# Optimization experiments

Measured on AMD Instinct MI355X. Metric: run time of the kernel, lower is better.

Reference implementation:

```python
import jax, jax.numpy as jnp
import numpy as np

HIDDEN_DIM = 128
ATTN_DIM = 64
B, N = 2, 512

def setup_inputs() -> dict:
    key = jax.random.key(0)
    ks = jax.random.split(key, 8)
    s = 0.05
    return {
        "X":    jax.random.normal(ks[0], (B, N, HIDDEN_DIM), dtype=jnp.float32),
        "Wo":   jax.random.normal(ks[1], (ATTN_DIM, HIDDEN_DIM), dtype=jnp.float32) * s,
        "W1":   jax.random.normal(ks[2], (ATTN_DIM, HIDDEN_DIM), dtype=jnp.float32) * s,
        "Wphi": jax.random.normal(ks[3], (ATTN_DIM,), dtype=jnp.float32) * s,
        "Wy":   jax.random.normal(ks[4], (HIDDEN_DIM, HIDDEN_DIM), dtype=jnp.float32) * s,
        "by":   jax.random.normal(ks[5], (HIDDEN_DIM,), dtype=jnp.float32) * s,
        "We":   jax.random.normal(ks[6], (HIDDEN_DIM, ATTN_DIM), dtype=jnp.float32) * s,
        "be":   jax.random.normal(ks[7], (HIDDEN_DIM,), dtype=jnp.float32) * s,
    }

def reference(X, Wo, W1, Wphi, Wy, by, We, be):
    # h_o, h_1: [B, N, A]
    h_o = jnp.einsum('bnc,ac->bna', X, Wo)
    h_1 = jnp.einsum('bnc,ac->bna', X, W1)
    # pairwise tanh edge features e_ij: [B, N, N, A]
    e = jnp.tanh(h_o[:, :, None, :] + h_1[:, None, :, :])
    # scores [B, N, N] via w_phi projection, row-wise softmax over j
    scores = jnp.einsum('bija,a->bij', e, Wphi)
    alpha = jax.nn.softmax(scores, axis=-1)
    # value path 1: Wy x_j -> aggregated by alpha (bmm)
    X_y = jnp.einsum('bnc,hc->bnh', X, Wy) + by
    part1 = jnp.einsum('bij,bjh->bih', alpha, X_y)
    # value path 2: We e_ij -> weighted sum over j
    eval_ = jnp.einsum('bija,ha->bijh', e, We) + be  # [B, N, N, H]
    part2 = jnp.einsum('bij,bijh->bih', alpha, eval_)
    return part1 + part2
```

## Files before the change

kernel.cpp:

```cpp
#include <hip/hip_runtime.h>

#define B_ 2
#define N_ 512
#define C_ 128
#define A_ 64
#define H_ 128

#define SC2L 2.885390081777927f
#define NEG2LE -2.885390081777927f

#define OFF_WOT 0
#define OFF_W1T (OFF_WOT + C_*A_)
#define OFF_WYT (OFF_W1T + C_*A_)
#define OFF_WET (OFF_WYT + C_*H_)
#define OFF_V   (OFF_WET + A_*H_)
#define OFF_UT2 (OFF_V   + B_*N_*A_)
#define OFF_USP (OFF_UT2 + B_*N_*A_/2)
#define OFF_XYP (OFF_USP + B_*N_*A_/2)

__device__ __forceinline__ float fexp2(float x) { return __builtin_amdgcn_exp2f(x); }
__device__ __forceinline__ float frcp(float x)  { return __builtin_amdgcn_rcpf(x); }
__device__ __forceinline__ unsigned f2bf(float x) {
  unsigned u = __float_as_uint(x);
  return (u + 0x7fffu + ((u >> 16) & 1u)) >> 16;
}
__device__ __forceinline__ float bf_lo(unsigned d) { return __uint_as_float(d << 16); }
__device__ __forceinline__ float bf_hi(unsigned d) { return __uint_as_float(d & 0xffff0000u); }

__global__ __launch_bounds__(256) void prep_weights(
    const float* __restrict__ Wo, const float* __restrict__ W1,
    const float* __restrict__ Wy, const float* __restrict__ We,
    float* __restrict__ ws) {
  int t = blockIdx.x * 256 + threadIdx.x;
  if (t < A_*C_) {
    int a = t / C_, c = t % C_;
    ws[OFF_WOT + c*A_ + a] = Wo[t];
    ws[OFF_W1T + c*A_ + a] = W1[t];
    int h2 = t / A_, a2 = t % A_;
    ws[OFF_WET + a2*H_ + h2] = We[t];
  }
  if (t < H_*C_) {
    int h = t / C_, c = t % C_;
    ws[OFF_WYT + c*H_ + h] = Wy[t];
  }
}

__global__ __launch_bounds__(256) void proj_kernel(
    const float* __restrict__ X, const float* __restrict__ by,
    float* __restrict__ ws) {
  __shared__ float xs[2*C_];
  int row0 = blockIdx.x * 2;
  int t = threadIdx.x;
  if (t < 2*C_) xs[t] = X[(size_t)row0*C_ + t];
  __syncthreads();

  const float* wt;
  int col, stride;
  if (t < 64)       { wt = ws + OFF_WOT; col = t;       stride = A_; }
  else if (t < 128) { wt = ws + OFF_W1T; col = t - 64;  stride = A_; }
  else              { wt = ws + OFF_WYT; col = t - 128; stride = H_; }

  float acc0 = 0.f, acc1 = 0.f;
  #pragma unroll 8
  for (int c = 0; c < C_; ++c) {
    float wv = wt[c*stride + col];
    acc0 = fmaf(xs[c], wv, acc0);
    acc1 = fmaf(xs[C_ + c], wv, acc1);
  }

  int b = row0 >> 9, n0 = row0 & (N_-1);
  int k = n0 >> 1;

  if (t < 64) {
    float* o = ws + OFF_V + (size_t)row0*A_ + col;
    o[0] = fexp2(SC2L * acc0);
    o[A_] = fexp2(SC2L * acc1);
  } else if (t < 128) {
    int a = col;
    unsigned u0 = f2bf(fexp2(SC2L * acc0));
    unsigned u1 = f2bf(fexp2(SC2L * acc1));
    unsigned* usp = (unsigned*)(ws + OFF_USP);
    usp[(size_t)(b*(N_/2) + k)*A_ + a] = u0 | (u1 << 16);
    unsigned short* ut = (unsigned short*)(ws + OFF_UT2);
    size_t base = ((size_t)(b*(A_/2) + (a >> 1))*N_ + n0)*2 + (a & 1);
    ut[base] = (unsigned short)u0;
    ut[base + 2] = (unsigned short)u1;
  } else {
    int h = col;
    float bb = by[h];
    unsigned x0 = f2bf(acc0 + bb);
    unsigned x1 = f2bf(acc1 + bb);
    unsigned* xp = (unsigned*)(ws + OFF_XYP);
    xp[(size_t)(b*(N_/2) + k)*H_ + h] = x0 | (x1 << 16);
  }
}

__global__ __launch_bounds__(512) void attn_kernel(
    const float* __restrict__ Wphi, const float* __restrict__ be,
    const float* __restrict__ ws, float* __restrict__ out) {
  __shared__ __align__(16) float2 pk2[A_];
  __shared__ float sc[N_];
  __shared__ float reds[8];
  __shared__ float ebw[8][A_];
  __shared__ float ebar[A_];
  __shared__ float p1s[4][H_];

  int t = threadIdx.x;
  int w = t >> 6, lane = t & 63;
  int bi = blockIdx.x;
  int b = bi >> 9, i = bi & (N_-1);

  const unsigned* ut2 = (const unsigned*)(ws + OFF_UT2) + (size_t)b*(A_/2)*N_;
  const unsigned* usp = (const unsigned*)(ws + OFF_USP) + (size_t)b*(N_/2)*A_;
  const unsigned* xyp = (const unsigned*)(ws + OFF_XYP) + (size_t)b*(N_/2)*H_;
  const float* wet = ws + OFF_WET;

  if (t < A_) {
    pk2[t] = make_float2(ws[OFF_V + (size_t)(b*N_ + i)*A_ + t], Wphi[t]);
  }
  __syncthreads();

  float s = 0.f;
  {
    const unsigned* up = ut2 + t;
    const float4* pkq = (const float4*)pk2;
    #pragma unroll 8
    for (int a2 = 0; a2 < A_/2; ++a2) {
      unsigned d = up[(size_t)a2*N_];
      float u0 = bf_lo(d), u1 = bf_hi(d);
      float4 vw = pkq[a2];
      s = fmaf(vw.y, frcp(fmaf(vw.x, u0, 1.f)), s);
      s = fmaf(vw.w, frcp(fmaf(vw.z, u1, 1.f)), s);
    }
  }
  float p = fexp2(NEG2LE * s);
  sc[t] = p;
  float q = p;
  #pragma unroll
  for (int m = 1; m < 64; m <<= 1) q += __shfl_xor(q, m);
  if (lane == 0) reds[w] = q;
  __syncthreads();

  {
    float v = pk2[lane].x;
    const unsigned* up = usp + lane;
    float c = 0.f;
    #pragma unroll 8
    for (int kk = 0; kk < N_/16; ++kk) {
      int k = kk*8 + w;
      unsigned d = up[(size_t)k*A_];
      float u0 = bf_lo(d), u1 = bf_hi(d);
      float p0 = sc[2*k], p1 = sc[2*k + 1];
      c = fmaf(p0, frcp(fmaf(v, u0, 1.f)), c);
      c = fmaf(p1, frcp(fmaf(v, u1, 1.f)), c);
    }
    ebw[w][lane] = c;
  }

  {
    int h = t & 127, qd = t >> 7;
    const unsigned* xp = xyp + (size_t)(qd*64)*H_ + h;
    float d0 = 0.f;
    #pragma unroll 8
    for (int kc = 0; kc < 64; ++kc) {
      unsigned d = xp[(size_t)kc*H_];
      int j = (qd*64 + kc)*2;
      d0 = fmaf(sc[j],     bf_lo(d), d0);
      d0 = fmaf(sc[j + 1], bf_hi(d), d0);
    }
    p1s[qd][h] = d0;
  }
  __syncthreads();

  if (t < A_) {
    float e = 0.f;
    #pragma unroll
    for (int k = 0; k < 8; ++k) e += ebw[k][t];
    float l = 0.f;
    #pragma unroll
    for (int k = 0; k < 8; ++k) l += reds[k];
    ebar[t] = l - 2.0f*e;
  }
  __syncthreads();

  if (t < H_) {
    int h = t;
    float l = 0.f;
    #pragma unroll
    for (int k = 0; k < 8; ++k) l += reds[k];
    float acc = p1s[0][h] + p1s[1][h] + p1s[2][h] + p1s[3][h];
    float e2 = 0.f;
    #pragma unroll 8
    for (int a = 0; a < A_; ++a) e2 = fmaf(ebar[a], wet[a*H_ + h], e2);
    out[(size_t)bi*H_ + h] = (acc + e2) * frcp(l) + be[h];
  }
}

extern "C" void kernel_launch(void* const* d_in, const int* in_sizes, int n_in,
                              void* d_out, int out_size, void* d_ws, size_t ws_size,
                              hipStream_t stream) {
  const float* X    = (const float*)d_in[0];
  const float* Wo   = (const float*)d_in[1];
  const float* W1   = (const float*)d_in[2];
  const float* Wphi = (const float*)d_in[3];
  const float* Wy   = (const float*)d_in[4];
  const float* by   = (const float*)d_in[5];
  const float* We   = (const float*)d_in[6];
  const float* be   = (const float*)d_in[7];
  float* out = (float*)d_out;
  float* ws  = (float*)d_ws;

  hipLaunchKernelGGL(prep_weights, dim3(64), dim3(256), 0, stream, Wo, W1, Wy, We, ws);
  hipLaunchKernelGGL(proj_kernel, dim3(B_*N_/2), dim3(256), 0, stream, X, by, ws);
  hipLaunchKernelGGL(attn_kernel, dim3(B_*N_), dim3(512), 0, stream, Wphi, be, ws, out);
}
```

Measured before the change: 94.56 us.

## Repack bf16 intermediates into 8-wide tiles for 128-bit vector loads

```diff
diff --git a/kernel.cpp b/kernel.cpp
--- a/kernel.cpp
+++ b/kernel.cpp
@@ -14,9 +14,9 @@
 #define OFF_WYT (OFF_W1T + C_*A_)
 #define OFF_WET (OFF_WYT + C_*H_)
 #define OFF_V   (OFF_WET + A_*H_)
-#define OFF_UT2 (OFF_V   + B_*N_*A_)
-#define OFF_USP (OFF_UT2 + B_*N_*A_/2)
-#define OFF_XYP (OFF_USP + B_*N_*A_/2)
+#define OFF_UT8 (OFF_V   + B_*N_*A_)
+#define OFF_US8 (OFF_UT8 + B_*N_*A_/2)
+#define OFF_XYP (OFF_US8 + B_*N_*A_/2)
 
 __device__ __forceinline__ float fexp2(float x) { return __builtin_amdgcn_exp2f(x); }
 __device__ __forceinline__ float frcp(float x)  { return __builtin_amdgcn_rcpf(x); }
@@ -69,7 +69,6 @@
   }
 
   int b = row0 >> 9, n0 = row0 & (N_-1);
-  int k = n0 >> 1;
 
   if (t < 64) {
     float* o = ws + OFF_V + (size_t)row0*A_ + col;
@@ -79,58 +78,71 @@
     int a = col;
     unsigned u0 = f2bf(fexp2(SC2L * acc0));
     unsigned u1 = f2bf(fexp2(SC2L * acc1));
-    unsigned* usp = (unsigned*)(ws + OFF_USP);
-    usp[(size_t)(b*(N_/2) + k)*A_ + a] = u0 | (u1 << 16);
-    unsigned short* ut = (unsigned short*)(ws + OFF_UT2);
-    size_t base = ((size_t)(b*(A_/2) + (a >> 1))*N_ + n0)*2 + (a & 1);
-    ut[base] = (unsigned short)u0;
-    ut[base + 2] = (unsigned short)u1;
+    unsigned short* ut = (unsigned short*)(ws + OFF_UT8);
+    size_t bA = ((size_t)(b*8 + (a >> 3))*N_ + n0)*8 + (a & 7);
+    ut[bA] = (unsigned short)u0;
+    ut[bA + 8] = (unsigned short)u1;
+    unsigned short* us = (unsigned short*)(ws + OFF_US8);
+    size_t bC = ((size_t)(b*64 + (n0 >> 3))*A_ + a)*8 + (n0 & 7);
+    us[bC] = (unsigned short)u0;
+    us[bC + 1] = (unsigned short)u1;
   } else {
     int h = col;
     float bb = by[h];
     unsigned x0 = f2bf(acc0 + bb);
     unsigned x1 = f2bf(acc1 + bb);
     unsigned* xp = (unsigned*)(ws + OFF_XYP);
-    xp[(size_t)(b*(N_/2) + k)*H_ + h] = x0 | (x1 << 16);
+    xp[(size_t)(b*(N_/2) + (n0 >> 1))*H_ + h] = x0 | (x1 << 16);
   }
 }
 
 __global__ __launch_bounds__(512) void attn_kernel(
     const float* __restrict__ Wphi, const float* __restrict__ be,
     const float* __restrict__ ws, float* __restrict__ out) {
-  __shared__ __align__(16) float2 pk2[A_];
+  __shared__ __align__(16) float pkv[A_];
+  __shared__ __align__(16) float pkw[A_];
   __shared__ float sc[N_];
   __shared__ float reds[8];
   __shared__ float ebw[8][A_];
   __shared__ float ebar[A_];
-  __shared__ float p1s[4][H_];
+  __shared__ __align__(16) float p1s[16][H_];
 
   int t = threadIdx.x;
   int w = t >> 6, lane = t & 63;
   int bi = blockIdx.x;
   int b = bi >> 9, i = bi & (N_-1);
 
-  const unsigned* ut2 = (const unsigned*)(ws + OFF_UT2) + (size_t)b*(A_/2)*N_;
-  const unsigned* usp = (const unsigned*)(ws + OFF_USP) + (size_t)b*(N_/2)*A_;
-  const unsigned* xyp = (const unsigned*)(ws + OFF_XYP) + (size_t)b*(N_/2)*H_;
+  const uint4* ut8 = (const uint4*)((const unsigned short*)(ws + OFF_UT8))
+                     + (size_t)b*8*N_;
+  const uint4* us8 = (const uint4*)((const unsigned short*)(ws + OFF_US8))
+                     + (size_t)b*64*A_;
+  const uint4* xy4 = (const uint4*)((const unsigned*)(ws + OFF_XYP))
+                     + (size_t)b*(N_/2)*(H_/4);
   const float* wet = ws + OFF_WET;
 
   if (t < A_) {
-    pk2[t] = make_float2(ws[OFF_V + (size_t)(b*N_ + i)*A_ + t], Wphi[t]);
+    pkv[t] = ws[OFF_V + (size_t)(b*N_ + i)*A_ + t];
+    pkw[t] = Wphi[t];
   }
   __syncthreads();
 
   float s = 0.f;
   {
-    const unsigned* up = ut2 + t;
-    const float4* pkq = (const float4*)pk2;
-    #pragma unroll 8
-    for (int a2 = 0; a2 < A_/2; ++a2) {
-      unsigned d = up[(size_t)a2*N_];
-      float u0 = bf_lo(d), u1 = bf_hi(d);
-      float4 vw = pkq[a2];
-      s = fmaf(vw.y, frcp(fmaf(vw.x, u0, 1.f)), s);
-      s = fmaf(vw.w, frcp(fmaf(vw.z, u1, 1.f)), s);
+    const float4* pv4 = (const float4*)pkv;
+    const float4* pw4 = (const float4*)pkw;
+    #pragma unroll
+    for (int g = 0; g < 8; ++g) {
+      uint4 d = ut8[(size_t)g*N_ + t];
+      float4 v0 = pv4[2*g], v1 = pv4[2*g + 1];
+      float4 w0 = pw4[2*g], w1 = pw4[2*g + 1];
+      s = fmaf(w0.x, frcp(fmaf(v0.x, bf_lo(d.x), 1.f)), s);
+      s = fmaf(w0.y, frcp(fmaf(v0.y, bf_hi(d.x), 1.f)), s);
+      s = fmaf(w0.z, frcp(fmaf(v0.z, bf_lo(d.y), 1.f)), s);
+      s = fmaf(w0.w, frcp(fmaf(v0.w, bf_hi(d.y), 1.f)), s);
+      s = fmaf(w1.x, frcp(fmaf(v1.x, bf_lo(d.z), 1.f)), s);
+      s = fmaf(w1.y, frcp(fmaf(v1.y, bf_hi(d.z), 1.f)), s);
+      s = fmaf(w1.z, frcp(fmaf(v1.z, bf_lo(d.w), 1.f)), s);
+      s = fmaf(w1.w, frcp(fmaf(v1.w, bf_hi(d.w), 1.f)), s);
     }
   }
   float p = fexp2(NEG2LE * s);
@@ -142,33 +154,40 @@
   __syncthreads();
 
   {
-    float v = pk2[lane].x;
-    const unsigned* up = usp + lane;
+    float v = pkv[lane];
+    const float4* sc4 = (const float4*)sc;
     float c = 0.f;
-    #pragma unroll 8
-    for (int kk = 0; kk < N_/16; ++kk) {
-      int k = kk*8 + w;
-      unsigned d = up[(size_t)k*A_];
-      float u0 = bf_lo(d), u1 = bf_hi(d);
-      float p0 = sc[2*k], p1 = sc[2*k + 1];
-      c = fmaf(p0, frcp(fmaf(v, u0, 1.f)), c);
-      c = fmaf(p1, frcp(fmaf(v, u1, 1.f)), c);
+    #pragma unroll
+    for (int oo = 0; oo < 8; ++oo) {
+      int o = oo*8 + w;
+      uint4 d = us8[(size_t)o*A_ + lane];
+      float4 pA = sc4[o*2], pB = sc4[o*2 + 1];
+      c = fmaf(pA.x, frcp(fmaf(v, bf_lo(d.x), 1.f)), c);
+      c = fmaf(pA.y, frcp(fmaf(v, bf_hi(d.x), 1.f)), c);
+      c = fmaf(pA.z, frcp(fmaf(v, bf_lo(d.y), 1.f)), c);
+      c = fmaf(pA.w, frcp(fmaf(v, bf_hi(d.y), 1.f)), c);
+      c = fmaf(pB.x, frcp(fmaf(v, bf_lo(d.z), 1.f)), c);
+      c = fmaf(pB.y, frcp(fmaf(v, bf_hi(d.z), 1.f)), c);
+      c = fmaf(pB.z, frcp(fmaf(v, bf_lo(d.w), 1.f)), c);
+      c = fmaf(pB.w, frcp(fmaf(v, bf_hi(d.w), 1.f)), c);
     }
     ebw[w][lane] = c;
   }
 
   {
-    int h = t & 127, qd = t >> 7;
-    const unsigned* xp = xyp + (size_t)(qd*64)*H_ + h;
-    float d0 = 0.f;
-    #pragma unroll 8
-    for (int kc = 0; kc < 64; ++kc) {
-      unsigned d = xp[(size_t)kc*H_];
-      int j = (qd*64 + kc)*2;
-      d0 = fmaf(sc[j],     bf_lo(d), d0);
-      d0 = fmaf(sc[j + 1], bf_hi(d), d0);
+    int h4 = t & 31, qd = t >> 5;
+    float d0 = 0.f, d1 = 0.f, d2 = 0.f, d3 = 0.f;
+    #pragma unroll
+    for (int kc = 0; kc < 16; ++kc) {
+      int k = qd*16 + kc;
+      uint4 d = xy4[(size_t)k*(H_/4) + h4];
+      float pa = sc[2*k], pb = sc[2*k + 1];
+      d0 = fmaf(pa, bf_lo(d.x), d0); d0 = fmaf(pb, bf_hi(d.x), d0);
+      d1 = fmaf(pa, bf_lo(d.y), d1); d1 = fmaf(pb, bf_hi(d.y), d1);
+      d2 = fmaf(pa, bf_lo(d.z), d2); d2 = fmaf(pb, bf_hi(d.z), d2);
+      d3 = fmaf(pa, bf_lo(d.w), d3); d3 = fmaf(pb, bf_hi(d.w), d3);
     }
-    p1s[qd][h] = d0;
+    *(float4*)&p1s[qd][h4*4] = make_float4(d0, d1, d2, d3);
   }
   __syncthreads();
 
@@ -188,7 +207,9 @@
     float l = 0.f;
     #pragma unroll
     for (int k = 0; k < 8; ++k) l += reds[k];
-    float acc = p1s[0][h] + p1s[1][h] + p1s[2][h] + p1s[3][h];
+    float acc = 0.f;
+    #pragma unroll
+    for (int k = 0; k < 16; ++k) acc += p1s[k][h];
     float e2 = 0.f;
     #pragma unroll 8
     for (int a = 0; a < A_; ++a) e2 = fmaf(ebar[a], wet[a*H_ + h], e2);
```

Measured after the change: 92.48 us. 2.2% less time.
